# Optimization experiments

Hardware: AMD Instinct MI355X
Metric: run time of the kernel (lower is better)

## Reference

```python
import jax, jax.numpy as jnp
import numpy as np

# Dimensions (see shape_source): batch, tokens, input dim, attention feature dim, output dim
B, T, D_IN, D_ATTN, D_OUT = 8, 2048, 512, 8, 512
# Weight scale keeps Q,K entries ~N(0, 0.5^2) so scores**power stays finite in fp32
W_SCALE = 0.5 / np.sqrt(D_IN)


def setup_inputs() -> dict:
    key = jax.random.key(0)
    k1, k2, k3, k4 = jax.random.split(key, 4)
    Input = jax.random.normal(k1, (B, T, D_IN), dtype=jnp.float32)
    W_q = jax.random.normal(k2, (D_IN, D_ATTN), dtype=jnp.float32) * W_SCALE
    W_k = jax.random.normal(k3, (D_IN, D_ATTN), dtype=jnp.float32) * W_SCALE
    W_v = jax.random.normal(k4, (D_IN, D_OUT), dtype=jnp.float32) * W_SCALE
    return {"Input": Input, "W_q": W_q, "W_k": W_k, "W_v": W_v, "power": D_ATTN}


def reference(Input, W_q, W_k, W_v, power):
    # QKV projections (torch.mm applied per token)
    Q = jnp.einsum('btd,df->btf', Input, W_q)   # [B,T,D_ATTN]
    K = jnp.einsum('btd,df->btf', Input, W_k)   # [B,T,D_ATTN]
    V = jnp.einsum('btd,do->bto', Input, W_v)   # [B,T,D_OUT]
    # Non-standard score transform: elementwise power by Attention.Feature.Num
    scores = jnp.einsum('btf,bsf->bts', Q, K) ** power  # [B,T,T]
    A = jax.nn.softmax(scores, axis=2)
    # Weighted sum of values
    return jnp.einsum('bts,bso->bto', A, V)  # [B,T,D_OUT]
```

## Files before the change

### kernel.cpp

```cpp
#include <hip/hip_runtime.h>
#include <hip/hip_bf16.h>
#include <stdint.h>


typedef float f32x4_t __attribute__((ext_vector_type(4)));
typedef short s16x8_t __attribute__((ext_vector_type(8)));
typedef unsigned int u32;

static __device__ __forceinline__ unsigned short f2bf(float x){
  union { float f; u32 u; } v; v.f = x;
  return (unsigned short)((v.u + 0x7FFFu + ((v.u >> 16) & 1u)) >> 16);
}

static __device__ __forceinline__ u32 pk2bf(float a, float b){
  __hip_bfloat162 h = __float22bfloat162_rn(float2{a, b});
  union { __hip_bfloat162 h2; u32 u; } c; c.h2 = h;
  return c.u;
}

static __device__ __forceinline__ void gload16(const void* g, void* l){
  __builtin_amdgcn_global_load_lds((const __attribute__((address_space(1))) u32*)g,
                                   (__attribute__((address_space(3))) u32*)l, 16, 0, 0);
}

static __device__ __forceinline__ float dot8(const float* q, const float4& a, const float4& b){
  float s = q[0] * a.x;
  s = fmaf(q[1], a.y, s); s = fmaf(q[2], a.z, s); s = fmaf(q[3], a.w, s);
  s = fmaf(q[4], b.x, s); s = fmaf(q[5], b.y, s); s = fmaf(q[6], b.z, s);
  s = fmaf(q[7], b.w, s);
  return s;
}

__global__ __launch_bounds__(256) void k_wvT(const float* __restrict__ Wv,
                                             unsigned short* __restrict__ WvT){
  __shared__ __align__(16) float tile[64][68];
  const int t = threadIdx.x;
  const int dbase = (blockIdx.x >> 3) * 64;
  const int cbase = (blockIdx.x & 7) * 64;
  {
    const int dl = t >> 2, cq = (t & 3) * 16;
    const float* src = Wv + (size_t)(dbase + dl) * 512 + cbase + cq;
#pragma unroll
    for (int i = 0; i < 16; i += 4){
      float4 v = *(const float4*)(src + i);
      tile[dl][cq + i + 0] = v.x; tile[dl][cq + i + 1] = v.y;
      tile[dl][cq + i + 2] = v.z; tile[dl][cq + i + 3] = v.w;
    }
  }
  __syncthreads();
  const int cl = t >> 2, dq = (t & 3) * 16;
  __align__(16) unsigned short o[16];
#pragma unroll
  for (int i = 0; i < 16; ++i) o[i] = f2bf(tile[dq + i][cl]);
  unsigned short* dst = WvT + (size_t)(cbase + cl) * 512 + dbase + dq;
  *(uint4*)dst = *(const uint4*)o;
  *(uint4*)(dst + 8) = *(const uint4*)(o + 8);
}

__global__ __launch_bounds__(256) void k_fused(const float* __restrict__ In,
                                               const float* __restrict__ Wq,
                                               const float* __restrict__ Wk,
                                               const unsigned short* __restrict__ WvT,
                                               float* __restrict__ Qo,
                                               float* __restrict__ Ko,
                                               unsigned short* __restrict__ Vg){
  __shared__ __align__(16) char smem[65536];
  const int t = threadIdx.x;
  if (blockIdx.x < 1024){
    float* wt = (float*)smem;
    float* inT = (float*)(smem + 32768);
    const float* Inb = In + (size_t)blockIdx.x * 16 * 512;
#pragma unroll
    for (int i = 0; i < 8; ++i)
      gload16(Inb + (i * 256 + t) * 4, (char*)inT + (i * 256 + t) * 16);
#pragma unroll
    for (int i = 0; i < 16; i += 4){
      float4 vq = *(const float4*)(Wq + t * 16 + i);
      float4 vk = *(const float4*)(Wk + t * 16 + i);
      const float* pq = &vq.x;
      const float* pk = &vk.x;
#pragma unroll
      for (int j = 0; j < 4; ++j){
        int flat = t * 16 + i + j;
        int d = flat >> 3, f = flat & 7;
        wt[f * 512 + ((((d >> 2) ^ f) << 2) | (d & 3))] = pq[j];
        int fk = f + 8;
        wt[fk * 512 + ((((d >> 2) ^ (fk & 7)) << 2) | (d & 3))] = pk[j];
      }
    }
    __syncthreads();
    const int tokl = t >> 4;
    const int f = t & 15;
    const float* inrow = inT + tokl * 512;
    const float* wrow = &wt[f * 512];
    const int swz = f & 7;
    double acc = 0.0;
    for (int cb = 0; cb < 128; cb += 8){
      float part = 0.f;
#pragma unroll
      for (int c = cb; c < cb + 8; ++c){
        float4 x = *(const float4*)(inrow + c * 4);
        float4 ww = *(const float4*)(wrow + ((c ^ swz) << 2));
        part = fmaf(x.x, ww.x, part); part = fmaf(x.y, ww.y, part);
        part = fmaf(x.z, ww.z, part); part = fmaf(x.w, ww.w, part);
      }
      acc += (double)part;
    }
    float r = (float)acc;
    const int tok = (int)blockIdx.x * 16 + tokl;
    if (f < 8) Qo[(size_t)tok * 8 + f] = r;
    else       Ko[(size_t)tok * 8 + (f - 8)] = r;
    return;
  }
  char* Ab = smem;
  char* Bb = smem + 16384;
  char* Img = smem + 32768;
  const int vb = (int)blockIdx.x - 1024;
  const int w = t >> 6, lane = t & 63;
  const int mt = vb >> 2, nt = vb & 3;
  const int wm = w >> 1, wn = w & 1;
  const int asub = lane & 3;
  int arow[2], acr[2];
#pragma unroll
  for (int i = 0; i < 2; ++i){
    arow[i] = (w * 2 + i) * 16 + (lane >> 2);
    acr[i]  = asub ^ ((arow[i] >> 1) & 3);
  }
  f32x4_t acc[4][4];
#pragma unroll
  for (int m = 0; m < 4; ++m)
#pragma unroll
    for (int n = 0; n < 4; ++n)
      acc[m][n] = (f32x4_t){0.f, 0.f, 0.f, 0.f};

  auto stageB = [&](int kk, int sel){
#pragma unroll
    for (int i = 0; i < 2; ++i){
      int id = w * 2 + i;
      const unsigned short* gb = WvT + (size_t)(nt * 128 + arow[i]) * 512 + kk * 32 + acr[i] * 8;
      gload16(gb, Bb + sel * 8192 + id * 1024);
    }
  };
  auto loadA = [&](int kk, float4* x, float4* y){
#pragma unroll
    for (int i = 0; i < 2; ++i){
      const float* ga = In + (size_t)(mt * 128 + arow[i]) * 512 + kk * 32 + acr[i] * 8;
      x[i] = *(const float4*)ga;
      y[i] = *(const float4*)(ga + 4);
    }
  };
  auto writeA = [&](const float4* x, const float4* y, int sel){
#pragma unroll
    for (int i = 0; i < 2; ++i){
      __align__(16) unsigned short pk[8] = {
        f2bf(x[i].x), f2bf(x[i].y), f2bf(x[i].z), f2bf(x[i].w),
        f2bf(y[i].x), f2bf(y[i].y), f2bf(y[i].z), f2bf(y[i].w)};
      *(uint4*)(Ab + sel * 8192 + arow[i] * 64 + asub * 16) = *(const uint4*)pk;
    }
  };
  {
    float4 x[2], y[2];
    loadA(0, x, y);
    stageB(0, 0);
    writeA(x, y, 0);
    __syncthreads();
  }
  for (int kk = 0; kk < 16; ++kk){
    const int cur = kk & 1;
    float4 x[2], y[2];
    if (kk < 15){
      loadA(kk + 1, x, y);
      stageB(kk + 1, cur ^ 1);
    }
    s16x8_t a[4], bf[4];
#pragma unroll
    for (int m = 0; m < 4; ++m){
      int row = wm * 64 + m * 16 + (lane & 15);
      int chn = (lane >> 4) ^ ((row >> 1) & 3);
      a[m] = *(const s16x8_t*)(Ab + cur * 8192 + row * 64 + chn * 16);
    }
#pragma unroll
    for (int n = 0; n < 4; ++n){
      int col = wn * 64 + n * 16 + (lane & 15);
      int chn = (lane >> 4) ^ ((col >> 1) & 3);
      bf[n] = *(const s16x8_t*)(Bb + cur * 8192 + col * 64 + chn * 16);
    }
#pragma unroll
    for (int m = 0; m < 4; ++m)
#pragma unroll
      for (int n = 0; n < 4; ++n)
        acc[m][n] = __builtin_amdgcn_mfma_f32_16x16x32_bf16(a[m], bf[n], acc[m][n], 0, 0, 0);
    if (kk < 15) writeA(x, y, cur ^ 1);
    __syncthreads();
  }
#pragma unroll
  for (int m = 0; m < 4; ++m){
    const int ks2 = (wm * 2 + (m >> 1)) & 3;
    const int hi  = (m * 2 + ((lane >> 4) >> 1)) & 3;
    const int lo0 = ((lane >> 4) & 1) * 4;
#pragma unroll
    for (int n = 0; n < 4; ++n){
      const int g_loc = wn * 2 + (n >> 1);
      const int n2 = n & 1;
      const int cl = lane & 15;
      __align__(8) unsigned short pk2[4];
#pragma unroll
      for (int j = 0; j < 4; ++j) pk2[j] = f2bf(acc[m][n][j]);
      int boff = g_loc * 8192 + n2 * 4096 + ks2 * 1024 + hi * 256 + cl * 16 + lo0 * 2;
      *(uint2*)(Img + boff) = *(const uint2*)pk2;
    }
  }
  __syncthreads();
  const int bq = mt >> 4;
  const int kt = mt & 15;
#pragma unroll
  for (int i = 0; i < 8; ++i){
    int G = i * 256 + t;
    unsigned short* dst = Vg + (size_t)bq * 1048576 + (size_t)kt * 65536
                        + nt * 16384 + G * 8;
    *(uint4*)dst = *(const uint4*)(Img + G * 16);
  }
}

__global__ __launch_bounds__(1024, 4) void k_attn(const float* __restrict__ Qg,
                                                  const float* __restrict__ Kg,
                                                  const unsigned short* __restrict__ Vg,
                                                  float* __restrict__ Out){
  __shared__ __align__(16) char smem[102656];
  const int t = threadIdx.x;
  const int g = t >> 6, lane = t & 63;
  const int b = blockIdx.x & 7;
  const int qt = blockIdx.x >> 3;
  const int qbase = qt * 64;

  float qreg[8];
  {
    const float* Qp = Qg + (size_t)(b * 2048 + qbase + lane) * 8;
    float4 a = *(const float4*)Qp;
    float4 c = *(const float4*)(Qp + 4);
    qreg[0] = a.x; qreg[1] = a.y; qreg[2] = a.z; qreg[3] = a.w;
    qreg[4] = c.x; qreg[5] = c.y; qreg[6] = c.z; qreg[7] = c.w;
  }
  const float* Kp = Kg + (size_t)b * (2048 * 8);
  const unsigned short* Vb = Vg + (size_t)b * 1048576;
  char* Klds = smem;
  char* Pb = smem + 65536;
  float* red = (float*)(smem + 98304);
  float* fin = (float*)(smem + 102400);

#pragma unroll
  for (int i = 0; i < 4; ++i)
    gload16(Kp + (size_t)(i * 1024 + t) * 4, Klds + (i * 1024 + t) * 16);
  __syncthreads();

  float amax2 = 0.f;
  {
    const float* kbase = (const float*)Klds + (g * 8) * 8;
#pragma unroll 2
    for (int tt = 0; tt < 16; ++tt){
      const float* kb = kbase + tt * 1024;
#pragma unroll
      for (int j = 0; j < 8; ++j){
        float4 k0 = *(const float4*)(kb + j * 8);
        float4 k1 = *(const float4*)(kb + j * 8 + 4);
        float s = dot8(qreg, k0, k1);
        amax2 = fmaxf(amax2, s * s);
      }
    }
  }
  red[g * 64 + lane] = amax2;
  __syncthreads();
  float am = red[lane];
#pragma unroll
  for (int s = 1; s < 16; ++s) am = fmaxf(am, red[s * 64 + lane]);
  float mreg;
  { float s4 = am * am; mreg = s4 * s4; }
  const float LOG2E = 1.44269504f;
  const float me2 = mreg * LOG2E;
  float lp = 0.f;

  const int pswz = ((g ^ (lane & 15)) << 4);
  auto score = [&](int tt, int sel){
    const float* kb = (const float*)Klds + (tt * 128 + g * 8) * 8;
    uint4 pkd;
    u32* pw = &pkd.x;
#pragma unroll
    for (int jp = 0; jp < 4; ++jp){
      float e0, e1;
#pragma unroll
      for (int h = 0; h < 2; ++h){
        const int j = jp * 2 + h;
        float4 k0 = *(const float4*)(kb + j * 8);
        float4 k1 = *(const float4*)(kb + j * 8 + 4);
        float s = dot8(qreg, k0, k1);
        float s2 = s * s; float s4 = s2 * s2; float p = s4 * s4;
        float e = __builtin_amdgcn_exp2f(fmaf(p, LOG2E, -me2));
        lp += e;
        if (h == 0) e0 = e; else e1 = e;
      }
      pw[jp] = pk2bf(e0, e1);
    }
    *(uint4*)(Pb + sel * 16384 + lane * 256 + pswz) = pkd;
  };

  auto vload = [&](int tt, s16x8_t vf[2][4]){
    const unsigned short* vb = Vb + (size_t)tt * 65536 + g * 4096 + lane * 8;
#pragma unroll
    for (int n = 0; n < 2; ++n)
#pragma unroll
      for (int ks = 0; ks < 4; ++ks)
        vf[n][ks] = *(const s16x8_t*)(vb + n * 2048 + ks * 512);
  };

  f32x4_t acc[4][2];
#pragma unroll
  for (int mm = 0; mm < 4; ++mm)
#pragma unroll
    for (int n = 0; n < 2; ++n)
      acc[mm][n] = (f32x4_t){0.f, 0.f, 0.f, 0.f};

  auto mfma_tile = [&](int sel, s16x8_t vf[2][4]){
#pragma unroll
    for (int ks = 0; ks < 4; ++ks){
      s16x8_t a[4];
#pragma unroll
      for (int mm = 0; mm < 4; ++mm){
        int r = mm * 16 + (lane & 15);
        int slot = (ks * 4 + (lane >> 4)) ^ (r & 15);
        a[mm] = *(const s16x8_t*)(Pb + sel * 16384 + r * 256 + (slot << 4));
      }
      __builtin_amdgcn_s_setprio(1);
#pragma unroll
      for (int mm = 0; mm < 4; ++mm)
#pragma unroll
        for (int n = 0; n < 2; ++n)
          acc[mm][n] = __builtin_amdgcn_mfma_f32_16x16x32_bf16(a[mm], vf[n][ks], acc[mm][n], 0, 0, 0);
      __builtin_amdgcn_s_setprio(0);
    }
  };

  score(0, 0);
  s16x8_t vfA[2][4], vfB[2][4];
  vload(0, vfA);
  __syncthreads();

  for (int it = 0; it < 8; ++it){
    const int t0 = it * 2, t1 = it * 2 + 1;
    vload(t1, vfB);
    if (t0 + 1 < 16) score(t0 + 1, 1);
    mfma_tile(0, vfA);
    __syncthreads();
    if (t1 + 1 < 16){
      vload(t1 + 1, vfA);
      score(t1 + 1, 0);
    }
    mfma_tile(1, vfB);
    __syncthreads();
  }

  red[g * 64 + lane] = lp;
  __syncthreads();
  if (t < 64){
    float s = red[t];
#pragma unroll
    for (int s2 = 1; s2 < 16; ++s2) s += red[s2 * 64 + t];
    fin[t] = 1.f / s;
  }
  __syncthreads();

  float* img = (float*)smem;
#pragma unroll
  for (int mm = 0; mm < 4; ++mm){
    float linv[4];
#pragma unroll
    for (int j = 0; j < 4; ++j)
      linv[j] = fin[mm * 16 + ((lane >> 4) << 2) + j];
#pragma unroll
    for (int n = 0; n < 2; ++n){
      int colL = g * 32 + n * 16 + (lane & 15);
#pragma unroll
      for (int j = 0; j < 4; ++j){
        int r16 = ((lane >> 4) << 2) + j;
        img[r16 * 520 + colL] = acc[mm][n][j] * linv[j];
      }
    }
    __syncthreads();
#pragma unroll
    for (int i = 0; i < 2; ++i){
      int f4 = i * 1024 + t;
      int r16 = f4 >> 7, c4 = f4 & 127;
      float4 v = *(const float4*)(img + r16 * 520 + c4 * 4);
      *(float4*)(Out + (size_t)(b * 2048 + qbase + mm * 16 + r16) * 512 + c4 * 4) = v;
    }
    __syncthreads();
  }
}

extern "C" void kernel_launch(void* const* d_in, const int* in_sizes, int n_in,
                              void* d_out, int out_size, void* d_ws, size_t ws_size,
                              hipStream_t stream){
  const float* In = (const float*)d_in[0];
  const float* Wq = (const float*)d_in[1];
  const float* Wk = (const float*)d_in[2];
  const float* Wv = (const float*)d_in[3];
  char* ws = (char*)d_ws;
  unsigned short* WvT = (unsigned short*)(ws);
  float* Q            = (float*)(ws + 524288);
  float* K            = (float*)(ws + 1048576);
  unsigned short* Vg  = (unsigned short*)(ws + 1572864);
  float* Out = (float*)d_out;

  hipLaunchKernelGGL(k_wvT,   dim3(64),   dim3(256),  0, stream, Wv, WvT);
  hipLaunchKernelGGL(k_fused, dim3(1536), dim3(256),  0, stream, In, Wq, Wk, WvT, Q, K, Vg);
  hipLaunchKernelGGL(k_attn,  dim3(256),  dim3(1024), 0, stream, Q, K, Vg, Out);
}
```

Measured before the change: 118.0 us.

## Interleave next-tile score computation with MFMA steps and drop V register prefetch

The attention main loop becomes one loop over 16 key tiles. The score/exp work for the next tile is spread across the four k-steps of the current tile's MFMA sequence, so VALU and matrix work can overlap within a wave. V fragments are now loaded at the start of each tile instead of being double-buffered in registers one tile ahead. The launch-bounds occupancy hint is removed, which frees the register budget but exposes the V global-load latency inside each iteration.

```diff
diff --git a/kernel.cpp b/kernel.cpp
--- a/kernel.cpp
+++ b/kernel.cpp
@@ -222,10 +222,10 @@
   }
 }
 
-__global__ __launch_bounds__(1024, 4) void k_attn(const float* __restrict__ Qg,
-                                                  const float* __restrict__ Kg,
-                                                  const unsigned short* __restrict__ Vg,
-                                                  float* __restrict__ Out){
+__global__ __launch_bounds__(1024) void k_attn(const float* __restrict__ Qg,
+                                               const float* __restrict__ Kg,
+                                               const unsigned short* __restrict__ Vg,
+                                               float* __restrict__ Out){
   __shared__ __align__(16) char smem[102656];
   const int t = threadIdx.x;
   const int g = t >> 6, lane = t & 63;
@@ -280,10 +280,17 @@
   float lp = 0.f;
 
   const int pswz = ((g ^ (lane & 15)) << 4);
-  auto score = [&](int tt, int sel){
+
+  f32x4_t acc[4][2];
+#pragma unroll
+  for (int mm = 0; mm < 4; ++mm)
+#pragma unroll
+    for (int n = 0; n < 2; ++n)
+      acc[mm][n] = (f32x4_t){0.f, 0.f, 0.f, 0.f};
+
+  auto score_full = [&](int tt, int sel){
     const float* kb = (const float*)Klds + (tt * 128 + g * 8) * 8;
-    uint4 pkd;
-    u32* pw = &pkd.x;
+    uint4 pkd; u32* pw = &pkd.x;
 #pragma unroll
     for (int jp = 0; jp < 4; ++jp){
       float e0, e1;
@@ -303,25 +310,40 @@
     *(uint4*)(Pb + sel * 16384 + lane * 256 + pswz) = pkd;
   };
 
-  auto vload = [&](int tt, s16x8_t vf[2][4]){
-    const unsigned short* vb = Vb + (size_t)tt * 65536 + g * 4096 + lane * 8;
-#pragma unroll
-    for (int n = 0; n < 2; ++n)
-#pragma unroll
-      for (int ks = 0; ks < 4; ++ks)
-        vf[n][ks] = *(const s16x8_t*)(vb + n * 2048 + ks * 512);
-  };
-
-  f32x4_t acc[4][2];
-#pragma unroll
-  for (int mm = 0; mm < 4; ++mm)
-#pragma unroll
-    for (int n = 0; n < 2; ++n)
-      acc[mm][n] = (f32x4_t){0.f, 0.f, 0.f, 0.f};
-
-  auto mfma_tile = [&](int sel, s16x8_t vf[2][4]){
+  score_full(0, 0);
+  __syncthreads();
+
+  for (int tt = 0; tt < 16; ++tt){
+    const int sel = tt & 1;
+    s16x8_t vf[2][4];
+    {
+      const unsigned short* vb = Vb + (size_t)tt * 65536 + g * 4096 + lane * 8;
+#pragma unroll
+      for (int n = 0; n < 2; ++n)
+#pragma unroll
+        for (int ks = 0; ks < 4; ++ks)
+          vf[n][ks] = *(const s16x8_t*)(vb + n * 2048 + ks * 512);
+    }
+    const bool more = (tt + 1 < 16);
+    const float* kb = (const float*)Klds + (((tt + 1) & 15) * 128 + g * 8) * 8;
+    uint4 pkd; u32* pw = &pkd.x;
 #pragma unroll
     for (int ks = 0; ks < 4; ++ks){
+      if (more){
+        float e0, e1;
+#pragma unroll
+        for (int h = 0; h < 2; ++h){
+          const int j = ks * 2 + h;
+          float4 k0 = *(const float4*)(kb + j * 8);
+          float4 k1 = *(const float4*)(kb + j * 8 + 4);
+          float s = dot8(qreg, k0, k1);
+          float s2 = s * s; float s4 = s2 * s2; float p = s4 * s4;
+          float e = __builtin_amdgcn_exp2f(fmaf(p, LOG2E, -me2));
+          lp += e;
+          if (h == 0) e0 = e; else e1 = e;
+        }
+        pw[ks] = pk2bf(e0, e1);
+      }
       s16x8_t a[4];
 #pragma unroll
       for (int mm = 0; mm < 4; ++mm){
@@ -337,24 +359,8 @@
           acc[mm][n] = __builtin_amdgcn_mfma_f32_16x16x32_bf16(a[mm], vf[n][ks], acc[mm][n], 0, 0, 0);
       __builtin_amdgcn_s_setprio(0);
     }
-  };
-
-  score(0, 0);
-  s16x8_t vfA[2][4], vfB[2][4];
-  vload(0, vfA);
-  __syncthreads();
-
-  for (int it = 0; it < 8; ++it){
-    const int t0 = it * 2, t1 = it * 2 + 1;
-    vload(t1, vfB);
-    if (t0 + 1 < 16) score(t0 + 1, 1);
-    mfma_tile(0, vfA);
-    __syncthreads();
-    if (t1 + 1 < 16){
-      vload(t1 + 1, vfA);
-      score(t1 + 1, 0);
-    }
-    mfma_tile(1, vfB);
+    if (more)
+      *(uint4*)(Pb + (sel ^ 1) * 16384 + lane * 256 + pswz) = pkd;
     __syncthreads();
   }
 
```

Measured after the change: 99.17 us. -16.0%, faster.
